# Optimization experiments

Measured on AMD Instinct MI355X. Metric: run time of the kernel, lower is better.

Reference implementation:

```python
import jax, jax.numpy as jnp
import numpy as np

B, P, C = 1024, 64, 512  # batch, patnum, d_model(channels)
LN_EPS = 1e-5

def setup_inputs() -> dict:
    key = jax.random.key(0)
    k = jax.random.split(key, 5)
    s = 1.0 / np.sqrt(P)  # torch Linear default init scale
    x  = jax.random.normal(k[0], (B, P, C), dtype=jnp.float32)
    W1 = jax.random.uniform(k[1], (C, P, P), minval=-s, maxval=s, dtype=jnp.float32)
    b1 = jax.random.uniform(k[2], (C, P),   minval=-s, maxval=s, dtype=jnp.float32)
    W2 = jax.random.uniform(k[3], (C, P, P), minval=-s, maxval=s, dtype=jnp.float32)
    b2 = jax.random.uniform(k[4], (C, P),   minval=-s, maxval=s, dtype=jnp.float32)
    gamma = jnp.ones((C,), dtype=jnp.float32)   # LayerNorm weight
    beta  = jnp.zeros((C,), dtype=jnp.float32)  # LayerNorm bias
    return {"x": x, "W1": W1, "b1": b1, "W2": W2, "b2": b2, "gamma": gamma, "beta": beta}

def reference(x, W1, b1, W2, b2, gamma, beta):
    # Per-channel Linear over the patch dim, batched across channels.
    # torch Linear: y[q] = sum_p x[p] * W[q, p] + b[q]
    h = jnp.einsum('bpc,cqp->bqc', x, W1) + b1.T[None]          # [B, P, C]
    h = jax.nn.gelu(h, approximate=False)                        # exact GELU (torch default)
    o = jnp.einsum('bpc,cqp->bqc', h, W2) + b2.T[None]          # [B, P, C]
    # Dropout is identity in eval; residual + LayerNorm over channel dim.
    res = o + x
    mean = jnp.mean(res, axis=-1, keepdims=True)
    var = jnp.mean((res - mean) ** 2, axis=-1, keepdims=True)
    return (res - mean) * jax.lax.rsqrt(var + LN_EPS) * gamma + beta
```

## Files before the change

kernel.cpp:

```cpp
#include <hip/hip_runtime.h>
#include <cstdint>
#include <cstddef>

#define BB 1024
#define PP 64
#define CC 512
constexpr float LN_EPS = 1e-5f;

typedef short  s16x8 __attribute__((ext_vector_type(8)));
typedef float  f32x4 __attribute__((ext_vector_type(4)));
typedef unsigned int u32x2 __attribute__((ext_vector_type(2)));

__device__ __forceinline__ unsigned cvt_pk_bf16(float lo, float hi) {
    unsigned r;
    asm("v_cvt_pk_bf16_f32 %0, %1, %2" : "=v"(r) : "v"(lo), "v"(hi));
    return r;
}
__device__ __forceinline__ float bflo(unsigned u) { union { unsigned u; float f; } v; v.u = u << 16;          return v.f; }
__device__ __forceinline__ float bfhi(unsigned u) { union { unsigned u; float f; } v; v.u = u & 0xffff0000u;  return v.f; }

__device__ __forceinline__ s16x8 ldwf(const float* p) {
    float4 a = *(const float4*)p;
    float4 b = *(const float4*)(p + 4);
    union { s16x8 v; unsigned u[4]; } r;
    r.u[0] = cvt_pk_bf16(a.x, a.y);
    r.u[1] = cvt_pk_bf16(a.z, a.w);
    r.u[2] = cvt_pk_bf16(b.x, b.y);
    r.u[3] = cvt_pk_bf16(b.z, b.w);
    return r.v;
}

__device__ __forceinline__ float gelu_t(float t) {
    float sg = 1.5957691216f * (t + 0.044715f * t * t * t);
    return t / (1.0f + __expf(-sg));
}

__global__ __launch_bounds__(1024) void k_mix(
    const float* __restrict__ X,  const float* __restrict__ W1,
    const float* __restrict__ B1, const float* __restrict__ W2,
    const float* __restrict__ B2, float* __restrict__ OUT)
{
    __shared__ __align__(16) unsigned short XS[16 * 1160];
    __shared__ __align__(16) unsigned short HS[16 * 1152];
    __shared__ __align__(16) float          RS[16 * 1092];
    __shared__ __align__(16) float          BS[16 * 128];

    const int tid  = threadIdx.x;
    const int lane = tid & 63;
    const int wv   = tid >> 6;
    const int lb   = lane & 15;
    const int lq   = lane >> 4;

    const int gid = blockIdx.x;
    const int cg  = gid & 31;
    const int bt  = gid >> 5;
    const int c0  = cg * 16, b0 = bt * 128;
    const int c   = c0 + wv;

    const float* w1c = W1 + (size_t)c * 4096;
    const float* w2c = W2 + (size_t)c * 4096;
    const int wq = lb * 64 + lq * 8;
    s16x8 w1_0_0 = ldwf(w1c +    0 + wq), w1_0_1 = ldwf(w1c +    0 + wq + 32);
    s16x8 w1_1_0 = ldwf(w1c + 1024 + wq), w1_1_1 = ldwf(w1c + 1024 + wq + 32);
    s16x8 w1_2_0 = ldwf(w1c + 2048 + wq), w1_2_1 = ldwf(w1c + 2048 + wq + 32);
    s16x8 w1_3_0 = ldwf(w1c + 3072 + wq), w1_3_1 = ldwf(w1c + 3072 + wq + 32);
    s16x8 w2_0_0 = ldwf(w2c +    0 + wq), w2_0_1 = ldwf(w2c +    0 + wq + 32);
    s16x8 w2_1_0 = ldwf(w2c + 1024 + wq), w2_1_1 = ldwf(w2c + 1024 + wq + 32);
    s16x8 w2_2_0 = ldwf(w2c + 2048 + wq), w2_2_1 = ldwf(w2c + 2048 + wq + 32);
    s16x8 w2_3_0 = ldwf(w2c + 3072 + wq), w2_3_1 = ldwf(w2c + 3072 + wq + 32);

    BS[wv * 128 +      lane] = B1[c * 64 + lane];
    BS[wv * 128 + 64 + lane] = B2[c * 64 + lane];

    const unsigned short* xp = &XS[wv * 1160];
    unsigned short*       hp = &HS[wv * 1152];

    const int sc4 = tid & 3;
    const int sp2 = (tid >> 2) & 31;
    const int sbo = tid >> 7;

    float4 r0[2], r1[2];
    #pragma unroll
    for (int pass = 0; pass < 2; ++pass) {
        const float* src = X + ((size_t)(b0 + pass * 8 + sbo) * PP + 2 * sp2) * CC
                             + c0 + sc4 * 4;
        r0[pass] = *(const float4*)src;
        r1[pass] = *(const float4*)(src + CC);
    }

    for (int s = 0; s < 8; ++s) {
        const int bb = b0 + s * 16;

        #pragma unroll
        for (int pass = 0; pass < 2; ++pass) {
            int b = pass * 8 + sbo;
            *(unsigned*)&XS[(sc4 * 4 + 0) * 1160 + b * 72 + 2 * sp2] = cvt_pk_bf16(r0[pass].x, r1[pass].x);
            *(unsigned*)&XS[(sc4 * 4 + 1) * 1160 + b * 72 + 2 * sp2] = cvt_pk_bf16(r0[pass].y, r1[pass].y);
            *(unsigned*)&XS[(sc4 * 4 + 2) * 1160 + b * 72 + 2 * sp2] = cvt_pk_bf16(r0[pass].z, r1[pass].z);
            *(unsigned*)&XS[(sc4 * 4 + 3) * 1160 + b * 72 + 2 * sp2] = cvt_pk_bf16(r0[pass].w, r1[pass].w);
        }
        __syncthreads();

        if (s < 7) {
            #pragma unroll
            for (int pass = 0; pass < 2; ++pass) {
                const float* src = X + ((size_t)(bb + 16 + pass * 8 + sbo) * PP + 2 * sp2) * CC
                                     + c0 + sc4 * 4;
                r0[pass] = *(const float4*)src;
                r1[pass] = *(const float4*)(src + CC);
            }
        }

        s16x8 xf0 = *(const s16x8*)(xp + lb * 72 +  0 + lq * 8);
        s16x8 xf1 = *(const s16x8*)(xp + lb * 72 + 32 + lq * 8);

        #define DO1(mt) { \
            float4 bv = *(const float4*)&BS[wv * 128 + mt * 16 + lq * 4]; \
            f32x4 a = {bv.x, bv.y, bv.z, bv.w}; \
            a = __builtin_amdgcn_mfma_f32_16x16x32_bf16(w1_##mt##_0, xf0, a, 0, 0, 0); \
            a = __builtin_amdgcn_mfma_f32_16x16x32_bf16(w1_##mt##_1, xf1, a, 0, 0, 0); \
            u32x2 h; \
            h[0] = cvt_pk_bf16(gelu_t(a[0]), gelu_t(a[1])); \
            h[1] = cvt_pk_bf16(gelu_t(a[2]), gelu_t(a[3])); \
            *(u32x2*)(hp + lb * 72 + mt * 16 + lq * 4) = h; }
        DO1(0) DO1(1) DO1(2) DO1(3)
        #undef DO1

        asm volatile("s_waitcnt lgkmcnt(0)" ::: "memory");

        s16x8 hf0 = *(const s16x8*)(hp + lb * 72 +  0 + lq * 8);
        s16x8 hf1 = *(const s16x8*)(hp + lb * 72 + 32 + lq * 8);

        #define DO2(mt) { \
            float4 bv = *(const float4*)&BS[wv * 128 + 64 + mt * 16 + lq * 4]; \
            f32x4 a = {bv.x, bv.y, bv.z, bv.w}; \
            a = __builtin_amdgcn_mfma_f32_16x16x32_bf16(w2_##mt##_0, hf0, a, 0, 0, 0); \
            a = __builtin_amdgcn_mfma_f32_16x16x32_bf16(w2_##mt##_1, hf1, a, 0, 0, 0); \
            u32x2 xv = *(const u32x2*)(xp + lb * 72 + mt * 16 + lq * 4); \
            a[0] += bflo(xv[0]); a[1] += bfhi(xv[0]); \
            a[2] += bflo(xv[1]); a[3] += bfhi(xv[1]); \
            *(f32x4*)&RS[lb * 1092 + wv * 68 + mt * 16 + lq * 4] = a; }
        DO2(0) DO2(1) DO2(2) DO2(3)
        #undef DO2
        __syncthreads();

        #pragma unroll
        for (int it = 0; it < 4; ++it) {
            int fi = it * 1024 + tid;
            int c4 = fi & 3, q = (fi >> 2) & 63, b = fi >> 8;
            const float* rp = &RS[b * 1092 + c4 * 4 * 68 + q];
            float4 v = { rp[0], rp[68], rp[136], rp[204] };
            *(float4*)(OUT + ((size_t)(bb + b) * PP + q) * CC + c0 + c4 * 4) = v;
        }
    }
}

__global__ __launch_bounds__(256) void k_ln(
    float* __restrict__ OUT, const float* __restrict__ G, const float* __restrict__ Be)
{
    const int lane = threadIdx.x & 63;
    const int m    = blockIdx.x * 4 + (threadIdx.x >> 6);
    float4* row = (float4*)(OUT + (size_t)m * CC);
    float4 v0 = row[lane], v1 = row[lane + 64];
    float s = (v0.x + v0.y) + (v0.z + v0.w) + (v1.x + v1.y) + (v1.z + v1.w);
    float q = (v0.x * v0.x + v0.y * v0.y) + (v0.z * v0.z + v0.w * v0.w)
            + (v1.x * v1.x + v1.y * v1.y) + (v1.z * v1.z + v1.w * v1.w);
    #pragma unroll
    for (int o = 32; o >= 1; o >>= 1) {
        s += __shfl_xor(s, o, 64);
        q += __shfl_xor(q, o, 64);
    }
    const float mu  = s * (1.0f / CC);
    const float var = q * (1.0f / CC) - mu * mu;
    const float inv = rsqrtf(var + LN_EPS);
    const float4 g0 = ((const float4*)G)[lane],  g1 = ((const float4*)G)[lane + 64];
    const float4 e0 = ((const float4*)Be)[lane], e1 = ((const float4*)Be)[lane + 64];
    v0.x = (v0.x - mu) * inv * g0.x + e0.x;  v0.y = (v0.y - mu) * inv * g0.y + e0.y;
    v0.z = (v0.z - mu) * inv * g0.z + e0.z;  v0.w = (v0.w - mu) * inv * g0.w + e0.w;
    v1.x = (v1.x - mu) * inv * g1.x + e1.x;  v1.y = (v1.y - mu) * inv * g1.y + e1.y;
    v1.z = (v1.z - mu) * inv * g1.z + e1.z;  v1.w = (v1.w - mu) * inv * g1.w + e1.w;
    row[lane] = v0; row[lane + 64] = v1;
}

extern "C" void kernel_launch(void* const* d_in, const int* in_sizes, int n_in,
                              void* d_out, int out_size, void* d_ws, size_t ws_size,
                              hipStream_t stream) {
    const float* X  = (const float*)d_in[0];
    const float* W1 = (const float*)d_in[1];
    const float* B1 = (const float*)d_in[2];
    const float* W2 = (const float*)d_in[3];
    const float* B2 = (const float*)d_in[4];
    const float* G  = (const float*)d_in[5];
    const float* Be = (const float*)d_in[6];
    float* OUT = (float*)d_out;

    k_mix<<<256, 1024, 0, stream>>>(X, W1, B1, W2, B2, OUT);
    k_ln<<<(BB * PP) / 4, 256, 0, stream>>>(OUT, G, Be);
}
```

Measured before the change: 340.3 us.

## Split mix kernel into 8-channel blocks with XCD-aware mapping and register biases

Halves the channel group per block (512 threads, 8 channels) and doubles the grid to 512 blocks, remapping block IDs so neighboring channel halves land on the same XCD. Biases move from LDS into registers, and residual x fragments are preloaded before the wait. Syncthreads is replaced by an explicit lgkmcnt wait plus s_barrier placed after the next X prefetch is issued. The aim is better occupancy and load balance across CUs, at the cost of more register pressure and narrower (32-byte) global writes per row segment.

```diff
diff --git a/kernel.cpp b/kernel.cpp
--- a/kernel.cpp
+++ b/kernel.cpp
@@ -35,15 +35,19 @@
     return t / (1.0f + __expf(-sg));
 }
 
-__global__ __launch_bounds__(1024) void k_mix(
+__device__ __forceinline__ void lds_barrier() {
+    asm volatile("s_waitcnt lgkmcnt(0)" ::: "memory");
+    __builtin_amdgcn_s_barrier();
+}
+
+__global__ __launch_bounds__(512, 4) void k_mix(
     const float* __restrict__ X,  const float* __restrict__ W1,
     const float* __restrict__ B1, const float* __restrict__ W2,
     const float* __restrict__ B2, float* __restrict__ OUT)
 {
-    __shared__ __align__(16) unsigned short XS[16 * 1160];
-    __shared__ __align__(16) unsigned short HS[16 * 1152];
-    __shared__ __align__(16) float          RS[16 * 1092];
-    __shared__ __align__(16) float          BS[16 * 128];
+    __shared__ __align__(16) unsigned short XS[8 * 1160];
+    __shared__ __align__(16) unsigned short HS[8 * 1152];
+    __shared__ __align__(16) float          RS[16 * 548];
 
     const int tid  = threadIdx.x;
     const int lane = tid & 63;
@@ -52,9 +56,12 @@
     const int lq   = lane >> 4;
 
     const int gid = blockIdx.x;
-    const int cg  = gid & 31;
-    const int bt  = gid >> 5;
-    const int c0  = cg * 16, b0 = bt * 128;
+    const int bt  = gid >> 6;
+    const int u   = gid & 63;
+    const int xcd = u & 7;
+    const int h   = (u >> 3) & 1;
+    const int cgp = xcd + (u >> 4) * 8;
+    const int c0  = cgp * 16 + h * 8, b0 = bt * 128;
     const int c   = c0 + wv;
 
     const float* w1c = W1 + (size_t)c * 4096;
@@ -68,16 +75,21 @@
     s16x8 w2_1_0 = ldwf(w2c + 1024 + wq), w2_1_1 = ldwf(w2c + 1024 + wq + 32);
     s16x8 w2_2_0 = ldwf(w2c + 2048 + wq), w2_2_1 = ldwf(w2c + 2048 + wq + 32);
     s16x8 w2_3_0 = ldwf(w2c + 3072 + wq), w2_3_1 = ldwf(w2c + 3072 + wq + 32);
-
-    BS[wv * 128 +      lane] = B1[c * 64 + lane];
-    BS[wv * 128 + 64 + lane] = B2[c * 64 + lane];
+    const float4 b1_0 = *(const float4*)(B1 + c * 64 +  0 + lq * 4);
+    const float4 b1_1 = *(const float4*)(B1 + c * 64 + 16 + lq * 4);
+    const float4 b1_2 = *(const float4*)(B1 + c * 64 + 32 + lq * 4);
+    const float4 b1_3 = *(const float4*)(B1 + c * 64 + 48 + lq * 4);
+    const float4 b2_0 = *(const float4*)(B2 + c * 64 +  0 + lq * 4);
+    const float4 b2_1 = *(const float4*)(B2 + c * 64 + 16 + lq * 4);
+    const float4 b2_2 = *(const float4*)(B2 + c * 64 + 32 + lq * 4);
+    const float4 b2_3 = *(const float4*)(B2 + c * 64 + 48 + lq * 4);
 
     const unsigned short* xp = &XS[wv * 1160];
     unsigned short*       hp = &HS[wv * 1152];
 
-    const int sc4 = tid & 3;
-    const int sp2 = (tid >> 2) & 31;
-    const int sbo = tid >> 7;
+    const int sc4 = tid & 1;
+    const int sp2 = (tid >> 1) & 31;
+    const int sbo = tid >> 6;
 
     float4 r0[2], r1[2];
     #pragma unroll
@@ -99,7 +111,6 @@
             *(unsigned*)&XS[(sc4 * 4 + 2) * 1160 + b * 72 + 2 * sp2] = cvt_pk_bf16(r0[pass].z, r1[pass].z);
             *(unsigned*)&XS[(sc4 * 4 + 3) * 1160 + b * 72 + 2 * sp2] = cvt_pk_bf16(r0[pass].w, r1[pass].w);
         }
-        __syncthreads();
 
         if (s < 7) {
             #pragma unroll
@@ -110,45 +121,48 @@
                 r1[pass] = *(const float4*)(src + CC);
             }
         }
+        lds_barrier();
 
         s16x8 xf0 = *(const s16x8*)(xp + lb * 72 +  0 + lq * 8);
         s16x8 xf1 = *(const s16x8*)(xp + lb * 72 + 32 + lq * 8);
 
         #define DO1(mt) { \
-            float4 bv = *(const float4*)&BS[wv * 128 + mt * 16 + lq * 4]; \
-            f32x4 a = {bv.x, bv.y, bv.z, bv.w}; \
+            f32x4 a = {b1_##mt.x, b1_##mt.y, b1_##mt.z, b1_##mt.w}; \
             a = __builtin_amdgcn_mfma_f32_16x16x32_bf16(w1_##mt##_0, xf0, a, 0, 0, 0); \
             a = __builtin_amdgcn_mfma_f32_16x16x32_bf16(w1_##mt##_1, xf1, a, 0, 0, 0); \
-            u32x2 h; \
-            h[0] = cvt_pk_bf16(gelu_t(a[0]), gelu_t(a[1])); \
-            h[1] = cvt_pk_bf16(gelu_t(a[2]), gelu_t(a[3])); \
-            *(u32x2*)(hp + lb * 72 + mt * 16 + lq * 4) = h; }
+            u32x2 hpk; \
+            hpk[0] = cvt_pk_bf16(gelu_t(a[0]), gelu_t(a[1])); \
+            hpk[1] = cvt_pk_bf16(gelu_t(a[2]), gelu_t(a[3])); \
+            *(u32x2*)(hp + lb * 72 + mt * 16 + lq * 4) = hpk; }
         DO1(0) DO1(1) DO1(2) DO1(3)
         #undef DO1
 
+        u32x2 xv0 = *(const u32x2*)(xp + lb * 72 +  0 + lq * 4);
+        u32x2 xv1 = *(const u32x2*)(xp + lb * 72 + 16 + lq * 4);
+        u32x2 xv2 = *(const u32x2*)(xp + lb * 72 + 32 + lq * 4);
+        u32x2 xv3 = *(const u32x2*)(xp + lb * 72 + 48 + lq * 4);
+
         asm volatile("s_waitcnt lgkmcnt(0)" ::: "memory");
 
         s16x8 hf0 = *(const s16x8*)(hp + lb * 72 +  0 + lq * 8);
         s16x8 hf1 = *(const s16x8*)(hp + lb * 72 + 32 + lq * 8);
 
         #define DO2(mt) { \
-            float4 bv = *(const float4*)&BS[wv * 128 + 64 + mt * 16 + lq * 4]; \
-            f32x4 a = {bv.x, bv.y, bv.z, bv.w}; \
+            f32x4 a = {b2_##mt.x, b2_##mt.y, b2_##mt.z, b2_##mt.w}; \
             a = __builtin_amdgcn_mfma_f32_16x16x32_bf16(w2_##mt##_0, hf0, a, 0, 0, 0); \
             a = __builtin_amdgcn_mfma_f32_16x16x32_bf16(w2_##mt##_1, hf1, a, 0, 0, 0); \
-            u32x2 xv = *(const u32x2*)(xp + lb * 72 + mt * 16 + lq * 4); \
-            a[0] += bflo(xv[0]); a[1] += bfhi(xv[0]); \
-            a[2] += bflo(xv[1]); a[3] += bfhi(xv[1]); \
-            *(f32x4*)&RS[lb * 1092 + wv * 68 + mt * 16 + lq * 4] = a; }
+            a[0] += bflo(xv##mt[0]); a[1] += bfhi(xv##mt[0]); \
+            a[2] += bflo(xv##mt[1]); a[3] += bfhi(xv##mt[1]); \
+            *(f32x4*)&RS[lb * 548 + wv * 68 + mt * 16 + lq * 4] = a; }
         DO2(0) DO2(1) DO2(2) DO2(3)
         #undef DO2
-        __syncthreads();
+        lds_barrier();
 
         #pragma unroll
         for (int it = 0; it < 4; ++it) {
-            int fi = it * 1024 + tid;
-            int c4 = fi & 3, q = (fi >> 2) & 63, b = fi >> 8;
-            const float* rp = &RS[b * 1092 + c4 * 4 * 68 + q];
+            int fi = it * 512 + tid;
+            int c4 = fi & 1, q = (fi >> 1) & 63, b = fi >> 7;
+            const float* rp = &RS[b * 548 + c4 * 272 + q];
             float4 v = { rp[0], rp[68], rp[136], rp[204] };
             *(float4*)(OUT + ((size_t)(bb + b) * PP + q) * CC + c0 + c4 * 4) = v;
         }
@@ -194,6 +208,6 @@
     const float* Be = (const float*)d_in[6];
     float* OUT = (float*)d_out;
 
-    k_mix<<<256, 1024, 0, stream>>>(X, W1, B1, W2, B2, OUT);
+    k_mix<<<512, 512, 0, stream>>>(X, W1, B1, W2, B2, OUT);
     k_ln<<<(BB * PP) / 4, 256, 0, stream>>>(OUT, G, Be);
 }
```

New measurement: 386.4 us. 1.14x slower.

## Write mix output channel-major to workspace and transpose inside LayerNorm kernel

Applied to the files above, without the earlier changes.

The mix kernel no longer stages results through shared memory for a transposed store. It writes residual outputs straight to a channel-major workspace buffer, optionally in fp16, and drops one block barrier per iteration. A new LayerNorm kernel reads 64 rows across all 512 channels, transposes them in LDS, reduces statistics, and writes the normalized output. This frees LDS and a sync in the mix kernel, but adds a full extra intermediate write and read pass through global memory. The original path is kept as a fallback when no workspace is available.

```diff
diff --git a/kernel.cpp b/kernel.cpp
--- a/kernel.cpp
+++ b/kernel.cpp
@@ -5,6 +5,7 @@
 #define BB 1024
 #define PP 64
 #define CC 512
+#define MM (BB * PP)
 constexpr float LN_EPS = 1e-5f;
 
 typedef short  s16x8 __attribute__((ext_vector_type(8)));
@@ -15,6 +16,16 @@
     unsigned r;
     asm("v_cvt_pk_bf16_f32 %0, %1, %2" : "=v"(r) : "v"(lo), "v"(hi));
     return r;
+}
+__device__ __forceinline__ unsigned cvt_pk_f16(float lo, float hi) {
+    unsigned r;
+    asm("v_cvt_pkrtz_f16_f32 %0, %1, %2" : "=v"(r) : "v"(lo), "v"(hi));
+    return r;
+}
+__device__ __forceinline__ float h2f(unsigned short h) {
+    float f;
+    asm("v_cvt_f32_f16 %0, %1" : "=v"(f) : "v"((unsigned)h));
+    return f;
 }
 __device__ __forceinline__ float bflo(unsigned u) { union { unsigned u; float f; } v; v.u = u << 16;          return v.f; }
 __device__ __forceinline__ float bfhi(unsigned u) { union { unsigned u; float f; } v; v.u = u & 0xffff0000u;  return v.f; }
@@ -35,14 +46,19 @@
     return t / (1.0f + __expf(-sg));
 }
 
-__global__ __launch_bounds__(1024) void k_mix(
+__device__ __forceinline__ void lds_barrier() {
+    asm volatile("s_waitcnt lgkmcnt(0)" ::: "memory");
+    __builtin_amdgcn_s_barrier();
+}
+
+template<int HALF>
+__global__ __launch_bounds__(1024, 4) void k_mix_rt(
     const float* __restrict__ X,  const float* __restrict__ W1,
     const float* __restrict__ B1, const float* __restrict__ W2,
-    const float* __restrict__ B2, float* __restrict__ OUT)
+    const float* __restrict__ B2, void* __restrict__ RTv)
 {
     __shared__ __align__(16) unsigned short XS[16 * 1160];
     __shared__ __align__(16) unsigned short HS[16 * 1152];
-    __shared__ __align__(16) float          RS[16 * 1092];
     __shared__ __align__(16) float          BS[16 * 128];
 
     const int tid  = threadIdx.x;
@@ -99,7 +115,6 @@
             *(unsigned*)&XS[(sc4 * 4 + 2) * 1160 + b * 72 + 2 * sp2] = cvt_pk_bf16(r0[pass].z, r1[pass].z);
             *(unsigned*)&XS[(sc4 * 4 + 3) * 1160 + b * 72 + 2 * sp2] = cvt_pk_bf16(r0[pass].w, r1[pass].w);
         }
-        __syncthreads();
 
         if (s < 7) {
             #pragma unroll
@@ -110,6 +125,7 @@
                 r1[pass] = *(const float4*)(src + CC);
             }
         }
+        lds_barrier();
 
         s16x8 xf0 = *(const s16x8*)(xp + lb * 72 +  0 + lq * 8);
         s16x8 xf1 = *(const s16x8*)(xp + lb * 72 + 32 + lq * 8);
@@ -119,18 +135,210 @@
             f32x4 a = {bv.x, bv.y, bv.z, bv.w}; \
             a = __builtin_amdgcn_mfma_f32_16x16x32_bf16(w1_##mt##_0, xf0, a, 0, 0, 0); \
             a = __builtin_amdgcn_mfma_f32_16x16x32_bf16(w1_##mt##_1, xf1, a, 0, 0, 0); \
-            u32x2 h; \
-            h[0] = cvt_pk_bf16(gelu_t(a[0]), gelu_t(a[1])); \
-            h[1] = cvt_pk_bf16(gelu_t(a[2]), gelu_t(a[3])); \
-            *(u32x2*)(hp + lb * 72 + mt * 16 + lq * 4) = h; }
+            u32x2 hpk; \
+            hpk[0] = cvt_pk_bf16(gelu_t(a[0]), gelu_t(a[1])); \
+            hpk[1] = cvt_pk_bf16(gelu_t(a[2]), gelu_t(a[3])); \
+            *(u32x2*)(hp + lb * 72 + mt * 16 + lq * 4) = hpk; }
         DO1(0) DO1(1) DO1(2) DO1(3)
         #undef DO1
 
+        u32x2 xv0 = *(const u32x2*)(xp + lb * 72 +  0 + lq * 4);
+        u32x2 xv1 = *(const u32x2*)(xp + lb * 72 + 16 + lq * 4);
+        u32x2 xv2 = *(const u32x2*)(xp + lb * 72 + 32 + lq * 4);
+        u32x2 xv3 = *(const u32x2*)(xp + lb * 72 + 48 + lq * 4);
+
         asm volatile("s_waitcnt lgkmcnt(0)" ::: "memory");
 
         s16x8 hf0 = *(const s16x8*)(hp + lb * 72 +  0 + lq * 8);
         s16x8 hf1 = *(const s16x8*)(hp + lb * 72 + 32 + lq * 8);
 
+        const size_t rbase = (size_t)c * MM + (size_t)(bb + lb) * 64 + lq * 4;
+        #define DO2(mt) { \
+            float4 bv = *(const float4*)&BS[wv * 128 + 64 + mt * 16 + lq * 4]; \
+            f32x4 a = {bv.x, bv.y, bv.z, bv.w}; \
+            a = __builtin_amdgcn_mfma_f32_16x16x32_bf16(w2_##mt##_0, hf0, a, 0, 0, 0); \
+            a = __builtin_amdgcn_mfma_f32_16x16x32_bf16(w2_##mt##_1, hf1, a, 0, 0, 0); \
+            a[0] += bflo(xv##mt[0]); a[1] += bfhi(xv##mt[0]); \
+            a[2] += bflo(xv##mt[1]); a[3] += bfhi(xv##mt[1]); \
+            if constexpr (!HALF) { \
+                *(f32x4*)((float*)RTv + rbase + mt * 16) = a; \
+            } else { \
+                u32x2 hv; \
+                hv[0] = cvt_pk_f16(a[0], a[1]); \
+                hv[1] = cvt_pk_f16(a[2], a[3]); \
+                *(u32x2*)((unsigned short*)RTv + rbase + mt * 16) = hv; \
+            } }
+        DO2(0) DO2(1) DO2(2) DO2(3)
+        #undef DO2
+
+        lds_barrier();
+    }
+}
+
+template<int HALF>
+__global__ __launch_bounds__(1024, 4) void k_ln_rt(
+    const void* __restrict__ RTv, float* __restrict__ OUT,
+    const float* __restrict__ G,  const float* __restrict__ Be)
+{
+    __shared__ float S[64][516];
+    __shared__ float pS[16][64];
+    __shared__ float pQ[16][64];
+    __shared__ float mu_s[64], inv_s[64];
+    __shared__ float gS[512], bS[512];
+
+    const int tid = threadIdx.x;
+    const int colbase = blockIdx.x * 64;
+
+    if (tid < 512) gS[tid] = G[tid];
+    else           bS[tid - 512] = Be[tid - 512];
+
+    #pragma unroll
+    for (int pass = 0; pass < 8; ++pass) {
+        const int cc = pass * 64 + (tid >> 4);
+        const int ch = (tid & 15) * 4;
+        float v0, v1, v2, v3;
+        if constexpr (!HALF) {
+            f32x4 v = *(const f32x4*)((const float*)RTv + (size_t)cc * MM + colbase + ch);
+            v0 = v[0]; v1 = v[1]; v2 = v[2]; v3 = v[3];
+        } else {
+            u32x2 v = *(const u32x2*)((const unsigned short*)RTv + (size_t)cc * MM + colbase + ch);
+            v0 = h2f((unsigned short)(v[0] & 0xffff)); v1 = h2f((unsigned short)(v[0] >> 16));
+            v2 = h2f((unsigned short)(v[1] & 0xffff)); v3 = h2f((unsigned short)(v[1] >> 16));
+        }
+        S[ch + 0][cc] = v0; S[ch + 1][cc] = v1;
+        S[ch + 2][cc] = v2; S[ch + 3][cc] = v3;
+    }
+    __syncthreads();
+
+    const int col = tid >> 4;
+    const int cs  = tid & 15;
+    float sum = 0.f, sq = 0.f;
+    #pragma unroll
+    for (int j = 0; j < 32; ++j) {
+        float v = S[col][j * 16 + cs];
+        sum += v; sq += v * v;
+    }
+    pS[cs][col] = sum; pQ[cs][col] = sq;
+    __syncthreads();
+
+    if (tid < 64) {
+        float s = 0.f, q = 0.f;
+        #pragma unroll
+        for (int k = 0; k < 16; ++k) { s += pS[k][tid]; q += pQ[k][tid]; }
+        const float mu  = s * (1.0f / CC);
+        const float var = q * (1.0f / CC) - mu * mu;
+        mu_s[tid]  = mu;
+        inv_s[tid] = rsqrtf(var + LN_EPS);
+    }
+    __syncthreads();
+
+    const int pos = tid & 7;
+    const int hs  = (tid >> 3) & 1;
+    const float mu  = mu_s[col];
+    const float inv = inv_s[col];
+    float* orow = OUT + (size_t)(colbase + col) * CC;
+    #pragma unroll
+    for (int k = 0; k < 8; ++k) {
+        const int cc = hs * 256 + k * 32 + pos * 4;
+        f32x4 v = *(const f32x4*)&S[col][cc];
+        f32x4 o;
+        o[0] = (v[0] - mu) * inv * gS[cc + 0] + bS[cc + 0];
+        o[1] = (v[1] - mu) * inv * gS[cc + 1] + bS[cc + 1];
+        o[2] = (v[2] - mu) * inv * gS[cc + 2] + bS[cc + 2];
+        o[3] = (v[3] - mu) * inv * gS[cc + 3] + bS[cc + 3];
+        *(f32x4*)(orow + cc) = o;
+    }
+}
+
+__global__ __launch_bounds__(1024) void k_mix_legacy(
+    const float* __restrict__ X,  const float* __restrict__ W1,
+    const float* __restrict__ B1, const float* __restrict__ W2,
+    const float* __restrict__ B2, float* __restrict__ OUT)
+{
+    __shared__ __align__(16) unsigned short XS[16 * 1160];
+    __shared__ __align__(16) unsigned short HS[16 * 1152];
+    __shared__ __align__(16) float          RS[16 * 1092];
+    __shared__ __align__(16) float          BS[16 * 128];
+
+    const int tid  = threadIdx.x;
+    const int lane = tid & 63;
+    const int wv   = tid >> 6;
+    const int lb   = lane & 15;
+    const int lq   = lane >> 4;
+
+    const int gid = blockIdx.x;
+    const int cg  = gid & 31;
+    const int bt  = gid >> 5;
+    const int c0  = cg * 16, b0 = bt * 128;
+    const int c   = c0 + wv;
+
+    const float* w1c = W1 + (size_t)c * 4096;
+    const float* w2c = W2 + (size_t)c * 4096;
+    const int wq = lb * 64 + lq * 8;
+    s16x8 w1_0_0 = ldwf(w1c +    0 + wq), w1_0_1 = ldwf(w1c +    0 + wq + 32);
+    s16x8 w1_1_0 = ldwf(w1c + 1024 + wq), w1_1_1 = ldwf(w1c + 1024 + wq + 32);
+    s16x8 w1_2_0 = ldwf(w1c + 2048 + wq), w1_2_1 = ldwf(w1c + 2048 + wq + 32);
+    s16x8 w1_3_0 = ldwf(w1c + 3072 + wq), w1_3_1 = ldwf(w1c + 3072 + wq + 32);
+    s16x8 w2_0_0 = ldwf(w2c +    0 + wq), w2_0_1 = ldwf(w2c +    0 + wq + 32);
+    s16x8 w2_1_0 = ldwf(w2c + 1024 + wq), w2_1_1 = ldwf(w2c + 1024 + wq + 32);
+    s16x8 w2_2_0 = ldwf(w2c + 2048 + wq), w2_2_1 = ldwf(w2c + 2048 + wq + 32);
+    s16x8 w2_3_0 = ldwf(w2c + 3072 + wq), w2_3_1 = ldwf(w2c + 3072 + wq + 32);
+
+    BS[wv * 128 +      lane] = B1[c * 64 + lane];
+    BS[wv * 128 + 64 + lane] = B2[c * 64 + lane];
+
+    const unsigned short* xp = &XS[wv * 1160];
+    unsigned short*       hp = &HS[wv * 1152];
+
+    const int sc4 = tid & 3;
+    const int sp2 = (tid >> 2) & 31;
+    const int sbo = tid >> 7;
+
+    float4 r0[2], r1[2];
+    #pragma unroll
+    for (int pass = 0; pass < 2; ++pass) {
+        const float* src = X + ((size_t)(b0 + pass * 8 + sbo) * PP + 2 * sp2) * CC
+                             + c0 + sc4 * 4;
+        r0[pass] = *(const float4*)src;
+        r1[pass] = *(const float4*)(src + CC);
+    }
+
+    for (int s = 0; s < 8; ++s) {
+        const int bb = b0 + s * 16;
+        #pragma unroll
+        for (int pass = 0; pass < 2; ++pass) {
+            int b = pass * 8 + sbo;
+            *(unsigned*)&XS[(sc4 * 4 + 0) * 1160 + b * 72 + 2 * sp2] = cvt_pk_bf16(r0[pass].x, r1[pass].x);
+            *(unsigned*)&XS[(sc4 * 4 + 1) * 1160 + b * 72 + 2 * sp2] = cvt_pk_bf16(r0[pass].y, r1[pass].y);
+            *(unsigned*)&XS[(sc4 * 4 + 2) * 1160 + b * 72 + 2 * sp2] = cvt_pk_bf16(r0[pass].z, r1[pass].z);
+            *(unsigned*)&XS[(sc4 * 4 + 3) * 1160 + b * 72 + 2 * sp2] = cvt_pk_bf16(r0[pass].w, r1[pass].w);
+        }
+        __syncthreads();
+        if (s < 7) {
+            #pragma unroll
+            for (int pass = 0; pass < 2; ++pass) {
+                const float* src = X + ((size_t)(bb + 16 + pass * 8 + sbo) * PP + 2 * sp2) * CC
+                                     + c0 + sc4 * 4;
+                r0[pass] = *(const float4*)src;
+                r1[pass] = *(const float4*)(src + CC);
+            }
+        }
+        s16x8 xf0 = *(const s16x8*)(xp + lb * 72 +  0 + lq * 8);
+        s16x8 xf1 = *(const s16x8*)(xp + lb * 72 + 32 + lq * 8);
+        #define DO1(mt) { \
+            float4 bv = *(const float4*)&BS[wv * 128 + mt * 16 + lq * 4]; \
+            f32x4 a = {bv.x, bv.y, bv.z, bv.w}; \
+            a = __builtin_amdgcn_mfma_f32_16x16x32_bf16(w1_##mt##_0, xf0, a, 0, 0, 0); \
+            a = __builtin_amdgcn_mfma_f32_16x16x32_bf16(w1_##mt##_1, xf1, a, 0, 0, 0); \
+            u32x2 hpk; \
+            hpk[0] = cvt_pk_bf16(gelu_t(a[0]), gelu_t(a[1])); \
+            hpk[1] = cvt_pk_bf16(gelu_t(a[2]), gelu_t(a[3])); \
+            *(u32x2*)(hp + lb * 72 + mt * 16 + lq * 4) = hpk; }
+        DO1(0) DO1(1) DO1(2) DO1(3)
+        #undef DO1
+        asm volatile("s_waitcnt lgkmcnt(0)" ::: "memory");
+        s16x8 hf0 = *(const s16x8*)(hp + lb * 72 +  0 + lq * 8);
+        s16x8 hf1 = *(const s16x8*)(hp + lb * 72 + 32 + lq * 8);
         #define DO2(mt) { \
             float4 bv = *(const float4*)&BS[wv * 128 + 64 + mt * 16 + lq * 4]; \
             f32x4 a = {bv.x, bv.y, bv.z, bv.w}; \
@@ -143,7 +351,6 @@
         DO2(0) DO2(1) DO2(2) DO2(3)
         #undef DO2
         __syncthreads();
-
         #pragma unroll
         for (int it = 0; it < 4; ++it) {
             int fi = it * 1024 + tid;
@@ -155,7 +362,7 @@
     }
 }
 
-__global__ __launch_bounds__(256) void k_ln(
+__global__ __launch_bounds__(256) void k_ln_legacy(
     float* __restrict__ OUT, const float* __restrict__ G, const float* __restrict__ Be)
 {
     const int lane = threadIdx.x & 63;
@@ -194,6 +401,17 @@
     const float* Be = (const float*)d_in[6];
     float* OUT = (float*)d_out;
 
-    k_mix<<<256, 1024, 0, stream>>>(X, W1, B1, W2, B2, OUT);
-    k_ln<<<(BB * PP) / 4, 256, 0, stream>>>(OUT, G, Be);
-}
+    const size_t need32 = (size_t)CC * MM * sizeof(float);
+    const size_t need16 = (size_t)CC * MM * sizeof(unsigned short);
+
+    if (d_ws && ws_size >= need32) {
+        k_mix_rt<0><<<256, 1024, 0, stream>>>(X, W1, B1, W2, B2, d_ws);
+        k_ln_rt<0><<<MM / 64, 1024, 0, stream>>>(d_ws, OUT, G, Be);
+    } else if (d_ws && ws_size >= need16) {
+        k_mix_rt<1><<<256, 1024, 0, stream>>>(X, W1, B1, W2, B2, d_ws);
+        k_ln_rt<1><<<MM / 64, 1024, 0, stream>>>(d_ws, OUT, G, Be);
+    } else {
+        k_mix_legacy<<<256, 1024, 0, stream>>>(X, W1, B1, W2, B2, OUT);
+        k_ln_legacy<<<MM / 4, 256, 0, stream>>>(OUT, G, Be);
+    }
+}
```

Result: no change. 339.9 us (-0.1%).
